# Kernel optimization log

Hardware: AMD Instinct MI355X
Metric: run time of the kernel (lower is better)

Reference implementation:

```python
import jax, jax.numpy as jnp
import numpy as np


def conv2d(x, w, b=None, pad=0):
    # x: [N,C,H,W], w: [O,I,kh,kw] (cross-correlation, matches torch conv2d)
    out = jax.lax.conv_general_dilated(
        x, w, window_strides=(1, 1), padding=[(pad, pad), (pad, pad)],
        dimension_numbers=('NCHW', 'OIHW', 'NCHW'))
    if b is not None:
        out = out + b[None, :, None, None]
    return out


def se_block(f, w1, b1, w2, b2):
    # squeeze-excite: global avg pool -> 1x1 conv -> relu -> 1x1 conv -> sigmoid
    s = jnp.mean(f, axis=(2, 3), keepdims=True)
    s = jax.nn.relu(conv2d(s, w1, b1, pad=0))
    s = jax.nn.sigmoid(conv2d(s, w2, b2, pad=0))
    return f * s


def setup_inputs() -> dict:
    key = jax.random.key(0)
    ks = jax.random.split(key, 32)
    B, C, H, W = 8, 3, 128, 128
    F_, S, K = 128, 8, 72  # features, squeeze, n basis kernels
    rn = lambda k, shp, sc=0.05: (jax.random.normal(k, shp, dtype=jnp.float32) * sc)
    return {
        'x': jax.random.normal(ks[0], (B, C, H, W), dtype=jnp.float32),
        'w_head': rn(ks[1], (F_, C, 3, 3)), 'b_head': rn(ks[2], (F_,)),
        'w_h1a': rn(ks[3], (F_, F_, 3, 3)), 'b_h1a': rn(ks[4], (F_,)),
        'w_h1b': rn(ks[5], (F_, F_, 3, 3)), 'b_h1b': rn(ks[6], (F_,)),
        'du1_w1': rn(ks[7], (S, F_, 1, 1)), 'du1_b1': rn(ks[8], (S,)),
        'du1_w2': rn(ks[9], (F_, S, 1, 1)), 'du1_b2': rn(ks[10], (F_,)),
        'w_h2a': rn(ks[11], (F_, F_, 3, 3)), 'b_h2a': rn(ks[12], (F_,)),
        'w_h2b': rn(ks[13], (F_, F_, 3, 3)), 'b_h2b': rn(ks[14], (F_,)),
        'du2_w1': rn(ks[15], (S, F_, 1, 1)), 'du2_b1': rn(ks[16], (S,)),
        'du2_w2': rn(ks[17], (F_, S, 1, 1)), 'du2_b2': rn(ks[18], (F_,)),
        'w_tail': rn(ks[19], (K, F_, 3, 3)), 'b_tail': rn(ks[20], (K,)),
        'kernel': rn(ks[21], (K, 1, 5, 5), 0.2),  # fixed 72x5x5 basis
    }


def reference(x, w_head, b_head, w_h1a, b_h1a, w_h1b, b_h1b,
              du1_w1, du1_b1, du1_w2, du1_b2,
              w_h2a, b_h2a, w_h2b, b_h2b,
              du2_w1, du2_b1, du2_w2, du2_b2,
              w_tail, b_tail, kernel):
    B, C, H, W = x.shape
    K = kernel.shape[0]
    # trunk: head -> (conv relu)x2 -> SE -> (conv relu)x2 -> SE -> tail
    f = conv2d(x, w_head, b_head, pad=1)
    f = jax.nn.relu(conv2d(f, w_h1a, b_h1a, pad=1))
    f = jax.nn.relu(conv2d(f, w_h1b, b_h1b, pad=1))
    f = se_block(f, du1_w1, du1_b1, du1_w2, du1_b2)
    f = jax.nn.relu(conv2d(f, w_h2a, b_h2a, pad=1))
    f = jax.nn.relu(conv2d(f, w_h2b, b_h2b, pad=1))
    f = se_block(f, du2_w1, du2_b1, du2_w2, du2_b2)
    wgt = conv2d(f, w_tail, b_tail, pad=1).reshape(B, 1, K, H, W)
    # dynamic filtering: apply 72 fixed 5x5 basis kernels per channel, then
    # per-pixel weighted sum over the 72 basis responses
    xp = jnp.pad(x, ((0, 0), (0, 0), (2, 2), (2, 2)), mode='reflect')
    xp = xp.reshape(B * C, 1, H + 4, W + 4)
    x_com = conv2d(xp, kernel, None, pad=0).reshape(B, C, K, H, W)
    out = jnp.sum(wgt * x_com, axis=2)  # [B,3,H,W]
    return out
```

## Files before the change

kernel.cpp:

```cpp
#include <hip/hip_runtime.h>
#include <math.h>


typedef __attribute__((ext_vector_type(8))) short bf16x8;
typedef __attribute__((ext_vector_type(4))) float f32x4;

__device__ inline float bf2f(unsigned short u) {
    unsigned v = ((unsigned)u) << 16;
    return __builtin_bit_cast(float, v);
}
__device__ inline unsigned short f2bf(float f) {
    unsigned u = __builtin_bit_cast(unsigned, f);
    u += 0x7FFF + ((u >> 16) & 1);
    return (unsigned short)(u >> 16);
}

__global__ __launch_bounds__(256) void head_conv(
    const float* __restrict__ x, const float* __restrict__ w,
    const float* __restrict__ bias, unsigned short* __restrict__ out)
{
    __shared__ float wlds[216];
    __shared__ float tile[3][34 * 34];
    const int tid = threadIdx.x, cog = blockIdx.y, b = blockIdx.z;
    const int tile_y = (blockIdx.x >> 2) * 32, tile_x = (blockIdx.x & 3) * 32;

    if (tid < 216) {
        int co = tid & 7, rest = tid >> 3, tap = rest % 9, ci = rest / 9;
        wlds[tid] = w[((cog * 8 + co) * 3 + ci) * 9 + tap];
    }
    for (int idx = tid; idx < 3 * 34 * 34; idx += 256) {
        int ci = idx / 1156, rem = idx - ci * 1156;
        int r = rem / 34, c = rem - r * 34;
        int gy = tile_y - 1 + r, gx = tile_x - 1 + c;
        float v = 0.f;
        if ((unsigned)gy < 128u && (unsigned)gx < 128u)
            v = x[(((size_t)(b * 3 + ci)) << 14) + (gy << 7) + gx];
        tile[ci][rem] = v;
    }
    __syncthreads();

    const int ty = tid >> 4, tx = tid & 15, py = ty * 2;
    float acc[2][2][8];
    #pragma unroll
    for (int r = 0; r < 2; ++r)
        #pragma unroll
        for (int h = 0; h < 2; ++h)
            #pragma unroll
            for (int co = 0; co < 8; ++co) acc[r][h][co] = 0.f;

    #pragma unroll
    for (int ci = 0; ci < 3; ++ci) {
        #pragma unroll
        for (int ky = 0; ky < 3; ++ky) {
            #pragma unroll
            for (int kx = 0; kx < 3; ++kx) {
                const float* wp = wlds + (ci * 9 + ky * 3 + kx) * 8;
                float i00 = tile[ci][(py + ky) * 34 + tx + kx];
                float i01 = tile[ci][(py + ky) * 34 + tx + 16 + kx];
                float i10 = tile[ci][(py + 1 + ky) * 34 + tx + kx];
                float i11 = tile[ci][(py + 1 + ky) * 34 + tx + 16 + kx];
                #pragma unroll
                for (int co = 0; co < 8; ++co) {
                    float wv = wp[co];
                    acc[0][0][co] += i00 * wv;
                    acc[0][1][co] += i01 * wv;
                    acc[1][0][co] += i10 * wv;
                    acc[1][1][co] += i11 * wv;
                }
            }
        }
    }

    #pragma unroll
    for (int r = 0; r < 2; ++r) {
        #pragma unroll
        for (int h = 0; h < 2; ++h) {
            int gy = tile_y + py + r, gx = tile_x + tx + h * 16;
            bf16x8 pv;
            #pragma unroll
            for (int co = 0; co < 8; ++co)
                pv[co] = (short)f2bf(acc[r][h][co] + bias[cog * 8 + co]);
            *(bf16x8*)(out + (((((size_t)b << 14) + gy * 128 + gx)) << 7) + cog * 8) = pv;
        }
    }
}

template <int LM, int NTW, int NSPLIT, int DOMEAN, int TAILFUSE, int NTHREADS>
__global__ __launch_bounds__(NTHREADS, (NTHREADS == 512) ? 4 : 2) void conv_mfma(
    const unsigned short* __restrict__ in, const unsigned short* __restrict__ wT,
    size_t wstride, const float* __restrict__ bias, unsigned short* __restrict__ out,
    float* __restrict__ meanb, const float* __restrict__ x,
    const unsigned short* __restrict__ kb, float* __restrict__ outf,
    int Coutp, int Cout, int relu)
{
    __shared__ unsigned short lds[TAILFUSE ? 26624 : 20736];
    const int tid = threadIdx.x;
    const int b = blockIdx.y;
    const int row0 = (blockIdx.x >> 3) << 4;
    const int col0 = (blockIdx.x & 7) << 4;
    const int l = tid & 63, wv = tid >> 6;
    const int li = l & 15, lq = l >> 4;
    const int m_base = (wv / NSPLIT) * LM;
    const int n_base = (wv % NSPLIT) * NTW;
    const size_t inb = ((size_t)b) << 14;
    const unsigned short* wbase = wT + (size_t)b * wstride;

    f32x4 acc[LM][NTW];
    #pragma unroll
    for (int lm = 0; lm < LM; ++lm)
        #pragma unroll
        for (int nt = 0; nt < NTW; ++nt)
            acc[lm][nt] = (f32x4){0.f, 0.f, 0.f, 0.f};

    #pragma unroll 1
    for (int half = 0; half < 2; ++half) {
        __syncthreads();
        for (int u = tid; u < 2592; u += NTHREADS) {
            int px = u >> 3, g = u & 7;
            int hr = px / 18, hc = px - hr * 18;
            int gy = row0 - 1 + hr, gx = col0 - 1 + hc;
            bf16x8 v = {0, 0, 0, 0, 0, 0, 0, 0};
            if ((unsigned)gy < 128u && (unsigned)gx < 128u)
                v = *(const bf16x8*)(in + ((inb + (gy << 7) + gx) << 7) + half * 64 + g * 8);
            int p = g ^ (px & 7);
            *(bf16x8*)(lds + px * 64 + p * 8) = v;
        }
        __syncthreads();

        auto loadB = [&](bf16x8 (&dst)[NTW], int s) {
            int tap = s >> 1, kcl = s & 1;
            const unsigned short* p = wbase +
                (size_t)(tap * 4 + half * 2 + kcl) * (Coutp * 32) +
                (n_base * 16 + li) * 32 + lq * 8;
            #pragma unroll
            for (int nt = 0; nt < NTW; ++nt)
                dst[nt] = *(const bf16x8*)(p + nt * 512);
        };
        auto compute = [&](bf16x8 (&bf)[NTW], int s) {
            int tap = s >> 1, kcl = s & 1;
            int ky = tap / 3, kx = tap - ky * 3;
            int g = kcl * 4 + lq;
            #pragma unroll
            for (int lm = 0; lm < LM; ++lm) {
                int px = (m_base + lm + ky) * 18 + li + kx;
                bf16x8 af = *(const bf16x8*)(lds + px * 64 + ((g ^ (px & 7)) * 8));
                #pragma unroll
                for (int nt = 0; nt < NTW; ++nt)
                    acc[lm][nt] = __builtin_amdgcn_mfma_f32_16x16x32_bf16(
                        af, bf[nt], acc[lm][nt], 0, 0, 0);
            }
        };

        bf16x8 bufA[NTW], bufB[NTW];
        loadB(bufA, 0);
        #pragma unroll 1
        for (int it = 0; it < 18; it += 2) {
            loadB(bufB, it + 1);
            compute(bufA, it);
            if (it + 2 < 18) loadB(bufA, it + 2);
            compute(bufB, it + 1);
        }
    }

    float bv[NTW], msum[NTW];
    #pragma unroll
    for (int nt = 0; nt < NTW; ++nt) {
        int co = (n_base + nt) * 16 + li;
        bv[nt] = (co < Cout) ? bias[co] : 0.f;
        msum[nt] = 0.f;
    }

    if (TAILFUSE) {
        __syncthreads();
        #pragma unroll
        for (int lm = 0; lm < LM; ++lm) {
            int rowl = m_base + lm;
            #pragma unroll
            for (int r = 0; r < 4; ++r) {
                int coll = lq * 4 + r;
                #pragma unroll
                for (int nt = 0; nt < NTW; ++nt)
                    lds[(rowl * 16 + coll) * 104 + nt * 16 + li] =
                        f2bf(acc[lm][nt][r] + bv[nt]);
            }
        }
        {
            bf16x8 z = {0, 0, 0, 0, 0, 0, 0, 0};
            *(bf16x8*)(lds + tid * 104 + 80) = z;
            *(bf16x8*)(lds + tid * 104 + 88) = z;
        }
        __syncthreads();

        f32x4 eacc[4][2];
        #pragma unroll
        for (int mm = 0; mm < 4; ++mm)
            #pragma unroll
            for (int nt = 0; nt < 2; ++nt)
                eacc[mm][nt] = (f32x4){0.f, 0.f, 0.f, 0.f};
        #pragma unroll
        for (int s = 0; s < 3; ++s) {
            bf16x8 kbf[2];
            #pragma unroll
            for (int nt = 0; nt < 2; ++nt)
                kbf[nt] = *(const bf16x8*)(kb + ((s * 2 + nt) * 16 + li) * 32 + lq * 8);
            #pragma unroll
            for (int mm = 0; mm < 4; ++mm) {
                int px = (wv * 4 + mm) * 16 + li;
                bf16x8 pf = *(const bf16x8*)(lds + px * 104 + s * 32 + lq * 8);
                #pragma unroll
                for (int nt = 0; nt < 2; ++nt)
                    eacc[mm][nt] = __builtin_amdgcn_mfma_f32_16x16x32_bf16(
                        pf, kbf[nt], eacc[mm][nt], 0, 0, 0);
            }
        }
        __syncthreads();

        float* elds = (float*)lds;
        #pragma unroll
        for (int mm = 0; mm < 4; ++mm) {
            #pragma unroll
            for (int nt = 0; nt < 2; ++nt) {
                int i = nt * 16 + li;
                if (i < 25) {
                    #pragma unroll
                    for (int r = 0; r < 4; ++r) {
                        int px = (wv * 4 + mm) * 16 + lq * 4 + r;
                        elds[px * 33 + i] = eacc[mm][nt][r];
                    }
                }
            }
        }
        __syncthreads();

        const int h = row0 + (tid >> 4), w = col0 + (tid & 15);
        const int pix = h * 128 + w;
        float e[25];
        #pragma unroll
        for (int i = 0; i < 25; ++i) e[i] = elds[tid * 33 + i];

        int yy[5], xx[5];
        #pragma unroll
        for (int d = 0; d < 5; ++d) {
            int y = h - 2 + d;
            yy[d] = y < 0 ? -y : (y > 127 ? 254 - y : y);
            int xv = w - 2 + d;
            xx[d] = xv < 0 ? -xv : (xv > 127 ? 254 - xv : xv);
        }
        #pragma unroll
        for (int c = 0; c < 3; ++c) {
            const float* xc = x + ((size_t)(b * 3 + c) << 14);
            float s = 0.f;
            #pragma unroll
            for (int dy = 0; dy < 5; ++dy)
                #pragma unroll
                for (int dx = 0; dx < 5; ++dx)
                    s += e[dy * 5 + dx] * xc[yy[dy] * 128 + xx[dx]];
            outf[((size_t)(b * 3 + c) << 14) + pix] = s;
        }
        return;
    }

    #pragma unroll
    for (int lm = 0; lm < LM; ++lm) {
        int row = row0 + m_base + lm;
        #pragma unroll
        for (int r = 0; r < 4; ++r) {
            int col = col0 + lq * 4 + r;
            size_t pbase = (inb + row * 128 + col) * (size_t)Coutp;
            #pragma unroll
            for (int nt = 0; nt < NTW; ++nt) {
                float v = acc[lm][nt][r] + bv[nt];
                if (relu) v = fmaxf(v, 0.f);
                if (DOMEAN) msum[nt] += v;
                out[pbase + (n_base + nt) * 16 + li] = f2bf(v);
            }
        }
    }
    if (DOMEAN) {
        #pragma unroll
        for (int nt = 0; nt < NTW; ++nt) {
            float t = msum[nt];
            t += __shfl_xor(t, 16, 64);
            t += __shfl_xor(t, 32, 64);
            if (lq == 0)
                atomicAdd(&meanb[b * 128 + (n_base + nt) * 16 + li], t);
        }
    }
}

__device__ inline void wtrans_one(const float* w, unsigned short* wT,
                                  int Co, int Coutp, int idx)
{
    int ch = idx & 31;
    int rest = idx >> 5;
    int co = rest % Coutp;
    int slice = rest / Coutp;
    int kc = slice & 3, tap = slice >> 2;
    float v = (co < Co) ? w[((size_t)(co * 128 + kc * 32 + ch)) * 9 + tap] : 0.f;
    wT[idx] = f2bf(v);
}

__global__ __launch_bounds__(256) void wtrans6(
    const float* __restrict__ w0, const float* __restrict__ w1,
    const float* __restrict__ w2, const float* __restrict__ w3,
    const float* __restrict__ w4, const float* __restrict__ kern,
    unsigned short* __restrict__ t0, unsigned short* __restrict__ t1,
    unsigned short* __restrict__ t2, unsigned short* __restrict__ t3,
    unsigned short* __restrict__ t4, unsigned short* __restrict__ kb,
    float* __restrict__ meanz)
{
    int idx = blockIdx.x * 256 + threadIdx.x;
    int y = blockIdx.y;
    if (y < 4) {
        const float* w = y == 0 ? w0 : y == 1 ? w1 : y == 2 ? w2 : w3;
        unsigned short* t = y == 0 ? t0 : y == 1 ? t1 : y == 2 ? t2 : t3;
        wtrans_one(w, t, 128, 128, idx);
    } else if (y == 4) {
        if (idx < 9 * 4 * 80 * 32) wtrans_one(w4, t4, 72, 80, idx);
    } else {
        if (idx < 3072) {
            int lq = (idx & 31) >> 3, j = idx & 7;
            int row = idx >> 5;
            int li = row & 15, snt = row >> 4;
            int s = snt >> 1, nt = snt & 1;
            int co = s * 32 + lq * 8 + j, i = nt * 16 + li;
            float v = (co < 72 && i < 25) ? kern[co * 25 + i] : 0.f;
            kb[idx] = f2bf(v);
        }
        if (idx < 2048) meanz[idx] = 0.f;
    }
}

__global__ __launch_bounds__(256) void wscale8f(
    const unsigned short* __restrict__ wT, const float* __restrict__ meanb,
    const float* __restrict__ w1, const float* __restrict__ b1,
    const float* __restrict__ w2, const float* __restrict__ b2,
    unsigned short* __restrict__ out, int Coutp)
{
    const int b = blockIdx.y, c = threadIdx.x;
    __shared__ float h1[8];
    __shared__ float sl[128];
    if (c < 8) {
        float s = 0.f;
        for (int j = 0; j < 128; ++j) s += w1[c * 128 + j] * meanb[b * 128 + j];
        h1[c] = fmaxf(s * (1.f / 16384.f) + b1[c], 0.f);
    }
    __syncthreads();
    if (c < 128) {
        float s = b2[c];
        #pragma unroll
        for (int j = 0; j < 8; ++j) s += w2[c * 8 + j] * h1[j];
        sl[c] = 1.f / (1.f + expf(-s));
    }
    __syncthreads();
    int r = blockIdx.x * 256 + c;
    int ch = r & 31;
    int kc = ((r >> 5) / Coutp) & 3;
    out[(size_t)b * (9 * 4 * Coutp * 32) + r] = f2bf(bf2f(wT[r]) * sl[kc * 32 + ch]);
}

extern "C" void kernel_launch(void* const* d_in, const int* in_sizes, int n_in,
                              void* d_out, int out_size, void* d_ws, size_t ws_size,
                              hipStream_t stream)
{
    const float* x      = (const float*)d_in[0];
    const float* w_head = (const float*)d_in[1];
    const float* b_head = (const float*)d_in[2];
    const float* w_h1a  = (const float*)d_in[3];
    const float* b_h1a  = (const float*)d_in[4];
    const float* w_h1b  = (const float*)d_in[5];
    const float* b_h1b  = (const float*)d_in[6];
    const float* du1_w1 = (const float*)d_in[7];
    const float* du1_b1 = (const float*)d_in[8];
    const float* du1_w2 = (const float*)d_in[9];
    const float* du1_b2 = (const float*)d_in[10];
    const float* w_h2a  = (const float*)d_in[11];
    const float* b_h2a  = (const float*)d_in[12];
    const float* w_h2b  = (const float*)d_in[13];
    const float* b_h2b  = (const float*)d_in[14];
    const float* du2_w1 = (const float*)d_in[15];
    const float* du2_b1 = (const float*)d_in[16];
    const float* du2_w2 = (const float*)d_in[17];
    const float* du2_b2 = (const float*)d_in[18];
    const float* w_tail = (const float*)d_in[19];
    const float* b_tail = (const float*)d_in[20];
    const float* kern   = (const float*)d_in[21];
    float* out = (float*)d_out;

    unsigned short* fb0  = (unsigned short*)d_ws;
    unsigned short* fb1  = fb0 + 16777216;
    unsigned short* wt1  = fb1 + 16777216;
    unsigned short* wt2  = wt1 + 147456;
    unsigned short* wt3  = wt2 + 147456;
    unsigned short* wt4  = wt3 + 147456;
    unsigned short* wtt  = wt4 + 147456;
    unsigned short* wsa  = wtt + 92160;
    unsigned short* wst  = wsa + 8 * 147456;
    unsigned short* kbb  = wst + 8 * 92160;
    float* mean1  = (float*)(kbb + 3072);
    float* mean2  = mean1 + 1024;

    dim3 blk(256);
    dim3 blk2(512);
    wtrans6<<<dim3(576, 6), blk, 0, stream>>>(w_h1a, w_h1b, w_h2a, w_h2b, w_tail,
                                              kern, wt1, wt2, wt3, wt4, wtt, kbb,
                                              mean1);

    head_conv<<<dim3(16, 16, 8), blk, 0, stream>>>(x, w_head, b_head, fb0);

    dim3 cgrid(64, 8);
    conv_mfma<4, 4, 2, 0, 0, 512><<<cgrid, blk2, 0, stream>>>(
        fb0, wt1, 0, b_h1a, fb1, nullptr, nullptr, nullptr, nullptr, 128, 128, 1);
    conv_mfma<4, 4, 2, 1, 0, 512><<<cgrid, blk2, 0, stream>>>(
        fb1, wt2, 0, b_h1b, fb0, mean1, nullptr, nullptr, nullptr, 128, 128, 1);

    wscale8f<<<dim3(576, 8), blk, 0, stream>>>(wt3, mean1, du1_w1, du1_b1,
                                               du1_w2, du1_b2, wsa, 128);

    conv_mfma<4, 4, 2, 0, 0, 512><<<cgrid, blk2, 0, stream>>>(
        fb0, wsa, 147456, b_h2a, fb1, nullptr, nullptr, nullptr, nullptr, 128, 128, 1);
    conv_mfma<4, 4, 2, 1, 0, 512><<<cgrid, blk2, 0, stream>>>(
        fb1, wt4, 0, b_h2b, fb0, mean2, nullptr, nullptr, nullptr, 128, 128, 1);

    wscale8f<<<dim3(360, 8), blk, 0, stream>>>(wtt, mean2, du2_w1, du2_b1,
                                               du2_w2, du2_b2, wst, 80);

    conv_mfma<4, 5, 1, 0, 1, 256><<<cgrid, blk, 0, stream>>>(
        fb0, wst, 92160, b_tail, nullptr, nullptr, x, kbb, out, 80, 72, 0);
}
```

Measured before the change: 375.6 us.

## Add 32x32x16 MFMA conv kernel for trunk 3x3 convolutions

Adds a new conv_mfma32 kernel that computes the four 128-channel trunk 3x3 convolutions with 32x32x16 bf16 MFMA tiles and 256 threads per block, replacing the 512-thread 16x16 variant. It stages the input halo in LDS in two channel halves with an XOR swizzle and double-buffers weight fragments in registers. The larger MFMA shape is meant to raise compute density and cut LDS A-fragment reads per FLOP. The trade-offs are heavier register use (eight 16-float accumulators per lane), scalar bf16 stores in the epilogue, and the weight layout must match the new lane mapping. The remaining conv_mfma launch bound is also changed to 2 blocks per SM.

```diff
diff --git a/kernel.cpp b/kernel.cpp
--- a/kernel.cpp
+++ b/kernel.cpp
@@ -4,6 +4,7 @@
 
 typedef __attribute__((ext_vector_type(8))) short bf16x8;
 typedef __attribute__((ext_vector_type(4))) float f32x4;
+typedef __attribute__((ext_vector_type(16))) float f32x16;
 
 __device__ inline float bf2f(unsigned short u) {
     unsigned v = ((unsigned)u) << 16;
@@ -85,8 +86,128 @@
     }
 }
 
+template <int DOMEAN>
+__global__ __launch_bounds__(256, 2) void conv_mfma32(
+    const unsigned short* __restrict__ in, const unsigned short* __restrict__ wT,
+    size_t wstride, const float* __restrict__ bias, unsigned short* __restrict__ out,
+    float* __restrict__ meanb, int relu)
+{
+    __shared__ unsigned short lds[20736];
+    const int tid = threadIdx.x;
+    const int b = blockIdx.y;
+    const int row0 = (blockIdx.x >> 3) << 4;
+    const int col0 = (blockIdx.x & 7) << 4;
+    const int l = tid & 63, wv = tid >> 6;
+    const int l5 = l >> 5;
+    const int a31 = l & 31;
+    const int rl = a31 >> 4, cl = a31 & 15;
+    const int ms = wv >> 1, ns = wv & 1;
+    const size_t inb = ((size_t)b) << 14;
+    const unsigned short* wbase = wT + (size_t)b * wstride;
+    const int pxb = (ms * 8 + rl) * 18 + cl;
+
+    f32x16 acc[4][2];
+    #pragma unroll
+    for (int mm = 0; mm < 4; ++mm)
+        #pragma unroll
+        for (int nt = 0; nt < 2; ++nt)
+            #pragma unroll
+            for (int i = 0; i < 16; ++i) acc[mm][nt][i] = 0.f;
+
+    #pragma unroll 1
+    for (int half = 0; half < 2; ++half) {
+        __syncthreads();
+        for (int u = tid; u < 2592; u += 256) {
+            int px = u >> 3, g = u & 7;
+            int hr = px / 18, hc = px - hr * 18;
+            int gy = row0 - 1 + hr, gx = col0 - 1 + hc;
+            bf16x8 v = {0, 0, 0, 0, 0, 0, 0, 0};
+            if ((unsigned)gy < 128u && (unsigned)gx < 128u)
+                v = *(const bf16x8*)(in + ((inb + (gy << 7) + gx) << 7) + half * 64 + g * 8);
+            int p = g ^ (px & 7);
+            *(bf16x8*)(lds + px * 64 + p * 8) = v;
+        }
+        __syncthreads();
+
+        auto loadB = [&](bf16x8 (&dst)[2][2], int u) {
+            int tap = u >> 1, kp = u & 1;
+            const unsigned short* p = wbase +
+                (size_t)(tap * 4 + half * 2 + kp) * (128 * 32) +
+                ((ns * 2) * 32 + a31) * 32 + l5 * 8;
+            #pragma unroll
+            for (int nt = 0; nt < 2; ++nt)
+                #pragma unroll
+                for (int k2 = 0; k2 < 2; ++k2)
+                    dst[nt][k2] = *(const bf16x8*)(p + nt * 1024 + k2 * 16);
+        };
+        auto compute = [&](bf16x8 (&bf)[2][2], int u) {
+            int tap = u >> 1, kp = u & 1;
+            int ky = tap / 3, kx = tap - ky * 3;
+            int t0 = pxb + ky * 18 + kx;
+            #pragma unroll
+            for (int mm = 0; mm < 4; ++mm) {
+                int px = t0 + mm * 36;
+                int x7 = px & 7;
+                #pragma unroll
+                for (int k2 = 0; k2 < 2; ++k2) {
+                    int g = kp * 4 + k2 * 2 + l5;
+                    bf16x8 af = *(const bf16x8*)(lds + px * 64 + ((g ^ x7) * 8));
+                    #pragma unroll
+                    for (int nt = 0; nt < 2; ++nt)
+                        acc[mm][nt] = __builtin_amdgcn_mfma_f32_32x32x16_bf16(
+                            af, bf[nt][k2], acc[mm][nt], 0, 0, 0);
+                }
+            }
+        };
+
+        bf16x8 bufA[2][2], bufB[2][2];
+        loadB(bufA, 0);
+        #pragma unroll 1
+        for (int u = 0; u < 18; u += 2) {
+            loadB(bufB, u + 1);
+            compute(bufA, u);
+            if (u + 2 < 18) loadB(bufA, u + 2);
+            compute(bufB, u + 1);
+        }
+    }
+
+    float bv[2], msum[2];
+    #pragma unroll
+    for (int nt = 0; nt < 2; ++nt) {
+        bv[nt] = bias[(ns * 2 + nt) * 32 + a31];
+        msum[nt] = 0.f;
+    }
+
+    #pragma unroll
+    for (int mm = 0; mm < 4; ++mm) {
+        int gybase = row0 + ((ms * 4 + mm) << 1);
+        #pragma unroll
+        for (int r = 0; r < 16; ++r) {
+            int m = (r & 3) + ((r >> 2) << 3) + (l5 << 2);
+            int gy = gybase + (m >> 4), gx = col0 + (m & 15);
+            size_t pbase = (inb + (gy << 7) + gx) << 7;
+            #pragma unroll
+            for (int nt = 0; nt < 2; ++nt) {
+                float v = acc[mm][nt][r] + bv[nt];
+                if (relu) v = fmaxf(v, 0.f);
+                if (DOMEAN) msum[nt] += v;
+                out[pbase + (ns * 2 + nt) * 32 + a31] = f2bf(v);
+            }
+        }
+    }
+    if (DOMEAN) {
+        #pragma unroll
+        for (int nt = 0; nt < 2; ++nt) {
+            float t = msum[nt];
+            t += __shfl_xor(t, 32, 64);
+            if (l5 == 0)
+                atomicAdd(&meanb[b * 128 + (ns * 2 + nt) * 32 + a31], t);
+        }
+    }
+}
+
 template <int LM, int NTW, int NSPLIT, int DOMEAN, int TAILFUSE, int NTHREADS>
-__global__ __launch_bounds__(NTHREADS, (NTHREADS == 512) ? 4 : 2) void conv_mfma(
+__global__ __launch_bounds__(NTHREADS, 2) void conv_mfma(
     const unsigned short* __restrict__ in, const unsigned short* __restrict__ wT,
     size_t wstride, const float* __restrict__ bias, unsigned short* __restrict__ out,
     float* __restrict__ meanb, const float* __restrict__ x,
@@ -401,7 +522,6 @@
     float* mean2  = mean1 + 1024;
 
     dim3 blk(256);
-    dim3 blk2(512);
     wtrans6<<<dim3(576, 6), blk, 0, stream>>>(w_h1a, w_h1b, w_h2a, w_h2b, w_tail,
                                               kern, wt1, wt2, wt3, wt4, wtt, kbb,
                                               mean1);
@@ -409,18 +529,14 @@
     head_conv<<<dim3(16, 16, 8), blk, 0, stream>>>(x, w_head, b_head, fb0);
 
     dim3 cgrid(64, 8);
-    conv_mfma<4, 4, 2, 0, 0, 512><<<cgrid, blk2, 0, stream>>>(
-        fb0, wt1, 0, b_h1a, fb1, nullptr, nullptr, nullptr, nullptr, 128, 128, 1);
-    conv_mfma<4, 4, 2, 1, 0, 512><<<cgrid, blk2, 0, stream>>>(
-        fb1, wt2, 0, b_h1b, fb0, mean1, nullptr, nullptr, nullptr, 128, 128, 1);
+    conv_mfma32<0><<<cgrid, blk, 0, stream>>>(fb0, wt1, 0, b_h1a, fb1, nullptr, 1);
+    conv_mfma32<1><<<cgrid, blk, 0, stream>>>(fb1, wt2, 0, b_h1b, fb0, mean1, 1);
 
     wscale8f<<<dim3(576, 8), blk, 0, stream>>>(wt3, mean1, du1_w1, du1_b1,
                                                du1_w2, du1_b2, wsa, 128);
 
-    conv_mfma<4, 4, 2, 0, 0, 512><<<cgrid, blk2, 0, stream>>>(
-        fb0, wsa, 147456, b_h2a, fb1, nullptr, nullptr, nullptr, nullptr, 128, 128, 1);
-    conv_mfma<4, 4, 2, 1, 0, 512><<<cgrid, blk2, 0, stream>>>(
-        fb1, wt4, 0, b_h2b, fb0, mean2, nullptr, nullptr, nullptr, 128, 128, 1);
+    conv_mfma32<0><<<cgrid, blk, 0, stream>>>(fb0, wsa, 147456, b_h2a, fb1, nullptr, 1);
+    conv_mfma32<1><<<cgrid, blk, 0, stream>>>(fb1, wt4, 0, b_h2b, fb0, mean2, 1);
 
     wscale8f<<<dim3(360, 8), blk, 0, stream>>>(wtt, mean2, du2_w1, du2_b1,
                                                du2_w2, du2_b2, wst, 80);
```

After: 346.9 us. 1.08x faster.
